# Optimization experiments

Hardware: AMD Instinct MI355X
Metric: run time of the kernel (lower is better)

The kernel has to match this reference:

```python
import jax, jax.numpy as jnp
import numpy as np

D_MODEL = 1024


def pos_encoding(seq_len, d_model):
    # pos: [S,1], i: [d/2]
    pos = jnp.arange(seq_len, dtype=jnp.float32)[:, None]
    i = jnp.arange(0, d_model, 2, dtype=jnp.float32)
    angle_rates = 1.0 / jnp.power(10000.0, i / d_model)
    angle_rads = pos * angle_rates  # [S, d/2]
    # NOTE: original concatenates sin block then cos block (not interleaved)
    return jnp.concatenate([jnp.sin(angle_rads), jnp.cos(angle_rads)], axis=-1)  # [S, d]


def setup_inputs() -> dict:
    key = jax.random.key(0)
    ks = jax.random.split(key, 4)
    B, S, D = 4, 2048, D_MODEL
    scale = 1.0 / np.sqrt(D)
    x = jax.random.normal(ks[0], (B, S, D), dtype=jnp.float32)
    Wq = jax.random.normal(ks[1], (D, D), dtype=jnp.float32) * scale
    Wk = jax.random.normal(ks[2], (D, D), dtype=jnp.float32) * scale
    Wv = jax.random.normal(ks[3], (D, D), dtype=jnp.float32) * scale
    bq = jnp.zeros((D,), dtype=jnp.float32)
    bk = jnp.zeros((D,), dtype=jnp.float32)
    bv = jnp.zeros((D,), dtype=jnp.float32)
    return {"x": x, "Wq": Wq, "bq": bq, "Wk": Wk, "bk": bk, "Wv": Wv, "bv": bv}


def reference(x, Wq, bq, Wk, bk, Wv, bv):
    B, S, D = x.shape
    pe = pos_encoding(S, D)  # [S, D]
    h = x + pe[None, :, :]
    q = jnp.einsum('bsd,de->bse', h, Wq) + bq
    k = jnp.einsum('bsd,de->bse', h, Wk) + bk
    v = jnp.einsum('bsd,de->bse', h, Wv) + bv
    logits = jnp.einsum('bqd,bkd->bqk', q, k) / jnp.sqrt(jnp.float32(D))
    attn = jax.nn.softmax(logits, axis=-1)
    out = jnp.einsum('bqk,bkd->bqd', attn, v)
    return x + out
```

## Files before the change

kernel.cpp:

```cpp
#include <hip/hip_runtime.h>
#include <stdint.h>


#define AS1(p) ((__attribute__((address_space(1))) void*)(p))
#define AS3(p) ((__attribute__((address_space(3))) void*)(p))

typedef _Float16 f16x8 __attribute__((ext_vector_type(8)));
typedef _Float16 f16x4 __attribute__((ext_vector_type(4)));
typedef float f32x4 __attribute__((ext_vector_type(4)));

__global__ __launch_bounds__(256) void prep(const float* __restrict__ x,
                                            _Float16* __restrict__ h,
                                            const float* __restrict__ Wq,
                                            const float* __restrict__ Wk,
                                            const float* __restrict__ Wv,
                                            _Float16* __restrict__ Wt,
                                            float* __restrict__ rowsum) {
  const int bx = blockIdx.x;
  const int tid = threadIdx.x;
  if (bx < 8192) {
    const size_t e = ((size_t)bx * 256 + tid) * 4;
    const int d = (int)(e & 1023);
    const int s = (int)((e >> 10) & 2047);
    const float4 xv = *(const float4*)(x + e);
    const int half = d >> 9;
    const int j0 = d & 511;
    const float c = -0.017988946039016f;
    f16x4 o;
#pragma unroll
    for (int t = 0; t < 4; t++) {
      const float r = __expf((float)(j0 + t) * c);
      const float a = (float)s * r;
      const float p = half ? __cosf(a) : __sinf(a);
      const float xe = (t == 0) ? xv.x : (t == 1) ? xv.y : (t == 2) ? xv.z : xv.w;
      o[t] = (_Float16)(xe + p);
    }
    *(f16x4*)(h + e) = o;
  } else if (bx < 11264) {
    __shared__ float t[32][33];
    const int w = bx - 8192;
    const int z = w >> 10;
    const int rem = w & 1023;
    const int n0 = (rem & 31) * 32, k0 = (rem >> 5) * 32;
    const float* W = (z == 0) ? Wq : (z == 1) ? Wk : Wv;
    _Float16* o = Wt + (size_t)z * 1048576;
    const int tx = tid & 31, ty = tid >> 5;
#pragma unroll
    for (int i = ty; i < 32; i += 8)
      t[i][tx] = W[(size_t)(k0 + i) * 1024 + (n0 + tx)];
    __syncthreads();
#pragma unroll
    for (int i = ty; i < 32; i += 8)
      o[(size_t)(n0 + i) * 1024 + (k0 + tx)] = (_Float16)t[tx][i];
  } else {
    rowsum[(bx - 11264) * 256 + tid] = 0.f;
  }
}

#define RD_A(SET, S_)                                                         \
  {                                                                           \
    _Pragma("unroll") for (int fi = 0; fi < 4; fi++)                          \
      _Pragma("unroll") for (int kk = 0; kk < 2; kk++)                        \
        SET[fi * 2 + kk] = *(const f16x8*)&As[bb][kk][                        \
            (wr * 128 + (S_) * 64 + fi * 16 + l16) * 32 + quad * 8];          \
  }
#define RD_B(SET, S_)                                                         \
  {                                                                           \
    _Pragma("unroll") for (int fj = 0; fj < 2; fj++)                          \
      _Pragma("unroll") for (int kk = 0; kk < 2; kk++)                        \
        SET[fj * 2 + kk] = *(const f16x8*)&Bs[bb][kk][                        \
            (wc * 64 + (S_) * 32 + fj * 16 + l16) * 32 + quad * 8];           \
  }
#define MFMA16(ASET, BSET, MQ, NQ)                                            \
  {                                                                           \
    __builtin_amdgcn_s_setprio(1);                                            \
    _Pragma("unroll") for (int fi = 0; fi < 4; fi++)                          \
      _Pragma("unroll") for (int fj = 0; fj < 2; fj++)                        \
        _Pragma("unroll") for (int kk = 0; kk < 2; kk++)                      \
          acc[(MQ) * 4 + fi][(NQ) * 2 + fj] =                                 \
              __builtin_amdgcn_mfma_f32_16x16x32_f16(                         \
                  ASET[fi * 2 + kk], BSET[fj * 2 + kk],                       \
                  acc[(MQ) * 4 + fi][(NQ) * 2 + fj], 0, 0, 0);                \
    __builtin_amdgcn_s_setprio(0);                                            \
  }
#define PHASE_WAIT()                                                          \
  __builtin_amdgcn_s_barrier();                                               \
  asm volatile("s_waitcnt lgkmcnt(0)" ::: "memory");                          \
  __builtin_amdgcn_sched_barrier(0);

template <int MODE>
__global__ __launch_bounds__(512) void gemm256(
    const _Float16* __restrict__ A0, long long sA,
    const _Float16* __restrict__ B0, long long sB,
    void* __restrict__ C0, long long sC,
    const float* __restrict__ aux0, const float* __restrict__ aux1,
    const float* __restrict__ aux2, float* __restrict__ rowsum,
    _Float16* __restrict__ vT, const int K, const int N, const int ldc) {
  __shared__ __align__(16) _Float16 As[2][2][8192];
  __shared__ __align__(16) _Float16 Bs[2][2][8192];
  const int tid = threadIdx.x;
  const int bid = blockIdx.x;

  int z, bm0, bn0;
  if (MODE == 0) {
    const int w = (bid & 7) * 48 + (bid >> 3);
    const int m = w / 12, r = w - m * 12;
    z = r >> 2; bn0 = (r & 3) * 256; bm0 = m * 256;
  } else {
    const int w = (bid & 7) * 32 + (bid >> 3);
    z = w >> 6;
    const int r = w & 63;
    bm0 = (r >> 3) * 256; bn0 = (r & 7) * 256;
  }
  const _Float16* A = A0 + (size_t)z * sA;
  const _Float16* Bt = B0 + (size_t)z * sB;

  const _Float16* aS = A + (size_t)(bm0 + (tid >> 2)) * K + (tid & 3) * 8;
  const _Float16* bS = Bt + (size_t)(bn0 + (tid >> 2)) * K + (tid & 3) * 8;
  const size_t halfStep = (size_t)128 * K;

  auto stageA = [&](int X, int h) {
    const int b = X & 1;
    const _Float16* s = aS + (size_t)X * 64 + (size_t)h * halfStep;
    _Float16* d = &As[b][0][h * 4096 + tid * 8];
    __builtin_amdgcn_global_load_lds(AS1(s), AS3(d), 16, 0, 0);
    __builtin_amdgcn_global_load_lds(AS1(s + 32), AS3(d + 8192), 16, 0, 0);
  };
  auto stageB = [&](int X, int h) {
    const int b = X & 1;
    const _Float16* s = bS + (size_t)X * 64 + (size_t)h * halfStep;
    _Float16* d = &Bs[b][0][h * 4096 + tid * 8];
    __builtin_amdgcn_global_load_lds(AS1(s), AS3(d), 16, 0, 0);
    __builtin_amdgcn_global_load_lds(AS1(s + 32), AS3(d + 8192), 16, 0, 0);
  };

  const int lane = tid & 63, wave = tid >> 6;
  const int wr = wave >> 2, wc = wave & 3;
  const int quad = lane >> 4, l16 = lane & 15;

  f32x4 acc[8][4];
#pragma unroll
  for (int i = 0; i < 8; i++)
#pragma unroll
    for (int j = 0; j < 4; j++) {
      f32x4 zz = {0.f, 0.f, 0.f, 0.f};
      acc[i][j] = zz;
    }

  const int nt = K >> 6;

  stageA(0, 0); stageA(0, 1); stageB(0, 0); stageB(0, 1);
  stageA(1, 0); stageA(1, 1);
  asm volatile("s_waitcnt vmcnt(4)" ::: "memory");
  __builtin_amdgcn_s_barrier();

  f16x8 a0[8], a1[8], b0f[4], b1f[4];

  for (int T = 0; T < nt; ++T) {
    const int bb = T & 1;
    RD_A(a0, 0);
    RD_B(b0f, 0);
    if (T + 1 < nt) stageB(T + 1, 0);
    PHASE_WAIT();
    MFMA16(a0, b0f, 0, 0);
    __builtin_amdgcn_s_barrier();
    RD_A(a1, 1);
    if (T + 1 < nt) stageB(T + 1, 1);
    PHASE_WAIT();
    MFMA16(a1, b0f, 1, 0);
    __builtin_amdgcn_s_barrier();
    RD_B(b1f, 1);
    if (T + 2 < nt) stageA(T + 2, 0);
    PHASE_WAIT();
    MFMA16(a0, b1f, 0, 1);
    __builtin_amdgcn_s_barrier();
    if (T + 2 < nt) stageA(T + 2, 1);
    PHASE_WAIT();
    MFMA16(a1, b1f, 1, 1);
    if (T + 1 < nt) {
      if (T + 2 < nt) asm volatile("s_waitcnt vmcnt(4)" ::: "memory");
      else            asm volatile("s_waitcnt vmcnt(0)" ::: "memory");
      __builtin_amdgcn_s_barrier();
    }
  }

  const int rowb = bm0 + wr * 128 + quad * 4;
  const int colb = bn0 + wc * 64 + l16;
  if (MODE == 0) {
    const float* bias = (z == 0) ? aux0 : (z == 1) ? aux1 : aux2;
    if (z == 2) {
      const int b_ = rowb >> 11, sl = rowb & 2047;
      _Float16* vb = vT + (size_t)b_ * 2097152;
#pragma unroll
      for (int i = 0; i < 8; i++)
#pragma unroll
        for (int j = 0; j < 4; j++) {
          const int gn = colb + j * 16;
          const float bb2 = bias[gn];
          f16x4 o;
#pragma unroll
          for (int r = 0; r < 4; r++) o[r] = (_Float16)(acc[i][j][r] + bb2);
          *(f16x4*)&vb[(size_t)gn * 2048 + sl + i * 16] = o;
        }
    } else {
      _Float16* C = (_Float16*)C0 + (size_t)z * sC;
#pragma unroll
      for (int i = 0; i < 8; i++)
#pragma unroll
        for (int j = 0; j < 4; j++) {
          const int gn = colb + j * 16;
          const float bb2 = bias[gn];
#pragma unroll
          for (int r = 0; r < 4; r++)
            C[(size_t)(rowb + i * 16 + r) * N + gn] = (_Float16)(acc[i][j][r] + bb2);
        }
    }
  } else {
    _Float16* C = (_Float16*)C0 + (size_t)z * sC;
    float rs[4] = {0.f, 0.f, 0.f, 0.f};
#pragma unroll
    for (int i = 0; i < 8; i++)
#pragma unroll
      for (int j = 0; j < 4; j++) {
        const int gn = colb + j * 16;
        f16x4 o;
        float pj = 0.f;
#pragma unroll
        for (int r = 0; r < 4; r++) {
          const float e = __expf(acc[i][j][r] * 0.03125f);
          o[r] = (_Float16)e;
          pj += e;
        }
        rs[j] += pj;
        *(f16x4*)&C[(size_t)gn * ldc + rowb + i * 16] = o;
      }
#pragma unroll
    for (int j = 0; j < 4; j++) {
      float v = rs[j];
      v += __shfl_xor(v, 16);
      v += __shfl_xor(v, 32);
      if (quad == 0) atomicAdd(&rowsum[z * 2048 + colb + j * 16], v);
    }
  }
}

__global__ __launch_bounds__(256) void gemm_pv(
    const _Float16* __restrict__ A0, long long sA,
    const _Float16* __restrict__ B0, long long sB,
    float* __restrict__ C0, long long sC,
    const float* __restrict__ X0, const float* __restrict__ rowsum,
    long long sX, const int K, const int ldc) {
  __shared__ __align__(16) _Float16 As[4 * 4096];
  __shared__ __align__(16) _Float16 Bs[4 * 4096];
  const int tid = threadIdx.x;
  const int bid = blockIdx.x;

  const int c = bid & 7, t0 = bid >> 3;
  const int zx = (t0 & 3) * 8 + c;
  const int y = t0 >> 2;
  const int z = zx >> 3;
  const int bm0 = (zx & 7) * 128, bn0 = y * 128;

  const _Float16* A = A0 + (size_t)z * sA;
  const _Float16* Bt = B0 + (size_t)z * sB;

  const _Float16* a0 = A + (size_t)(bm0 + (tid >> 2)) * K + (tid & 3) * 8;
  const _Float16* a1 = a0 + (size_t)64 * K;
  const _Float16* b0 = Bt + (size_t)(bn0 + (tid >> 2)) * K + (tid & 3) * 8;
  const _Float16* b1 = b0 + (size_t)64 * K;

  auto stage = [&](int s) {
    const int r = s & 3;
    const int k = s * 32;
    __builtin_amdgcn_global_load_lds(AS1(a0 + k), AS3(&As[r * 4096 + tid * 8]), 16, 0, 0);
    __builtin_amdgcn_global_load_lds(AS1(a1 + k), AS3(&As[r * 4096 + tid * 8 + 2048]), 16, 0, 0);
    __builtin_amdgcn_global_load_lds(AS1(b0 + k), AS3(&Bs[r * 4096 + tid * 8]), 16, 0, 0);
    __builtin_amdgcn_global_load_lds(AS1(b1 + k), AS3(&Bs[r * 4096 + tid * 8 + 2048]), 16, 0, 0);
  };

  const int lane = tid & 63, wave = tid >> 6;
  const int wr = wave >> 1, wc = wave & 1;
  const int quad = lane >> 4, l16 = lane & 15;

  f32x4 acc[4][4];
#pragma unroll
  for (int i = 0; i < 4; i++)
#pragma unroll
    for (int j = 0; j < 4; j++) {
      f32x4 zz = {0.f, 0.f, 0.f, 0.f};
      acc[i][j] = zz;
    }

  const int NS = K >> 5;

  stage(0); stage(1); stage(2);
  asm volatile("s_waitcnt vmcnt(8)" ::: "memory");
  __builtin_amdgcn_s_barrier();

  for (int s = 0; s < NS; ++s) {
    const int r = s & 3;
    f16x8 af[4], bf[4];
#pragma unroll
    for (int i = 0; i < 4; i++)
      af[i] = *(const f16x8*)&As[r * 4096 + (wr * 64 + i * 16 + l16) * 32 + quad * 8];
#pragma unroll
    for (int j = 0; j < 4; j++)
      bf[j] = *(const f16x8*)&Bs[r * 4096 + (wc * 64 + j * 16 + l16) * 32 + quad * 8];
    if (s + 3 < NS) stage(s + 3);
    __builtin_amdgcn_s_barrier();
    asm volatile("s_waitcnt lgkmcnt(0)" ::: "memory");
    __builtin_amdgcn_sched_barrier(0);
    __builtin_amdgcn_s_setprio(1);
#pragma unroll
    for (int i = 0; i < 4; i++)
#pragma unroll
      for (int j = 0; j < 4; j++)
        acc[i][j] = __builtin_amdgcn_mfma_f32_16x16x32_f16(af[i], bf[j],
                                                           acc[i][j], 0, 0, 0);
    __builtin_amdgcn_s_setprio(0);
    __builtin_amdgcn_sched_barrier(0);
    if (s + 1 < NS) {
      if (s + 3 < NS)       asm volatile("s_waitcnt vmcnt(8)" ::: "memory");
      else if (s + 3 == NS) asm volatile("s_waitcnt vmcnt(4)" ::: "memory");
      else                  asm volatile("s_waitcnt vmcnt(0)" ::: "memory");
      __builtin_amdgcn_s_barrier();
    }
  }

  const int rowb = bm0 + wr * 64 + quad * 4;
  const int colb = bn0 + wc * 64 + l16;
  float* C = C0 + (size_t)z * sC;
  const float* X = X0 + (size_t)z * sX;
  float inv[4];
#pragma unroll
  for (int j = 0; j < 4; j++)
    inv[j] = 1.0f / rowsum[z * 2048 + colb + j * 16];
#pragma unroll
  for (int i = 0; i < 4; i++)
#pragma unroll
    for (int j = 0; j < 4; j++) {
      const int gn = colb + j * 16;
      const size_t base = (size_t)gn * ldc + rowb + i * 16;
      const float4 xv = *(const float4*)(X + base);
      float4 o;
      o.x = acc[i][j][0] * inv[j] + xv.x;
      o.y = acc[i][j][1] * inv[j] + xv.y;
      o.z = acc[i][j][2] * inv[j] + xv.z;
      o.w = acc[i][j][3] * inv[j] + xv.w;
      *(float4*)(C + base) = o;
    }
}

extern "C" void kernel_launch(void* const* d_in, const int* in_sizes, int n_in,
                              void* d_out, int out_size, void* d_ws, size_t ws_size,
                              hipStream_t stream) {
  (void)in_sizes; (void)n_in; (void)out_size; (void)ws_size;
  const float* x  = (const float*)d_in[0];
  const float* Wq = (const float*)d_in[1];
  const float* bq = (const float*)d_in[2];
  const float* Wk = (const float*)d_in[3];
  const float* bk = (const float*)d_in[4];
  const float* Wv = (const float*)d_in[5];
  const float* bv = (const float*)d_in[6];
  float* out = (float*)d_out;
  char* ws = (char*)d_ws;

  _Float16* h    = (_Float16*)(ws);
  _Float16* Wt   = (_Float16*)(ws + 16777216);
  _Float16* qkv  = (_Float16*)(ws + 23068672);
  _Float16* attn = (_Float16*)(ws + 73400320);
  float* rowsum  = (float*)   (ws + 106954752);

  const long long E = 8388608;
  _Float16* vT = qkv + 2 * E;

  prep<<<11296, 256, 0, stream>>>(x, h, Wq, Wk, Wv, Wt, rowsum);

  gemm256<0><<<384, 512, 0, stream>>>(
      h, 0LL, Wt, 1048576LL, qkv, E, bq, bk, bv, nullptr, vT,
      1024, 1024, 0);

  gemm256<1><<<256, 512, 0, stream>>>(
      qkv + E, 2097152LL, qkv, 2097152LL, attn, 4194304LL,
      nullptr, nullptr, nullptr, rowsum, nullptr,
      1024, 2048, 2048);

  gemm_pv<<<512, 256, 0, stream>>>(
      vT, 2097152LL, attn, 4194304LL, out, 2097152LL,
      x, rowsum, 2097152LL, 2048, 1024);
}
```

Before: 265.1 us.

## Replace QKV projection GEMM with dedicated 256x128-tile kernel using triple-buffered LDS

The QKV projection now runs in its own kernel with 256-thread blocks, 256x128 output tiles and a three-stage global-to-LDS ring buffer, launched as 768 blocks instead of 384 blocks of 512 threads with 256x256 tiles. The templated kernel is specialised to the logits-only path, and gemm_pv is moved without functional change. The aim is better occupancy and load balance across CUs on the projection GEMM. In exchange, each block reuses each loaded tile less and the new kernel drops the phased sub-tile pipelining of the old one.

```diff
diff --git a/kernel.cpp b/kernel.cpp
--- a/kernel.cpp
+++ b/kernel.cpp
@@ -57,6 +57,225 @@
   }
 }
 
+__global__ __launch_bounds__(256) void gemm_qkv(
+    const _Float16* __restrict__ A0, const _Float16* __restrict__ B0,
+    _Float16* __restrict__ qk, const float* __restrict__ bq,
+    const float* __restrict__ bk, const float* __restrict__ bv,
+    _Float16* __restrict__ vT) {
+  constexpr int K = 1024;
+  __shared__ __align__(16) _Float16 As[3 * 8192];
+  __shared__ __align__(16) _Float16 Bs[3 * 4096];
+  const int tid = threadIdx.x;
+  const int bid = blockIdx.x;
+
+  const int w = (bid & 7) * 96 + (bid >> 3);
+  const int m = w / 24, r = w - m * 24;
+  const int z = r >> 3, n = r & 7;
+  const int bm0 = m * 256, bn0 = n * 128;
+
+  const _Float16* Bt = B0 + (size_t)z * 1048576;
+  const _Float16* aS = A0 + (size_t)(bm0 + (tid >> 2)) * K + (tid & 3) * 8;
+  const _Float16* bS = Bt + (size_t)(bn0 + (tid >> 2)) * K + (tid & 3) * 8;
+
+  auto stage = [&](int kt, int ra, int rb2) {
+    const int k = kt * 32;
+    __builtin_amdgcn_global_load_lds(AS1(aS + k), AS3(&As[ra + tid * 8]), 16, 0, 0);
+    __builtin_amdgcn_global_load_lds(AS1(aS + k + 64 * K), AS3(&As[ra + tid * 8 + 2048]), 16, 0, 0);
+    __builtin_amdgcn_global_load_lds(AS1(aS + k + 128 * K), AS3(&As[ra + tid * 8 + 4096]), 16, 0, 0);
+    __builtin_amdgcn_global_load_lds(AS1(aS + k + 192 * K), AS3(&As[ra + tid * 8 + 6144]), 16, 0, 0);
+    __builtin_amdgcn_global_load_lds(AS1(bS + k), AS3(&Bs[rb2 + tid * 8]), 16, 0, 0);
+    __builtin_amdgcn_global_load_lds(AS1(bS + k + 64 * K), AS3(&Bs[rb2 + tid * 8 + 2048]), 16, 0, 0);
+  };
+
+  const int lane = tid & 63, wave = tid >> 6;
+  const int wr = wave >> 1, wc = wave & 1;
+  const int quad = lane >> 4, l16 = lane & 15;
+
+  f32x4 acc[8][4];
+#pragma unroll
+  for (int i = 0; i < 8; i++)
+#pragma unroll
+    for (int j = 0; j < 4; j++) {
+      f32x4 zz = {0.f, 0.f, 0.f, 0.f};
+      acc[i][j] = zz;
+    }
+
+  const int NS = K >> 5;
+
+  stage(0, 0, 0);
+  stage(1, 8192, 4096);
+  asm volatile("s_waitcnt vmcnt(6)" ::: "memory");
+  __builtin_amdgcn_s_barrier();
+
+  int rA = 0, rB = 0;
+  int sA = 16384, sB = 8192;
+  for (int s = 0; s < NS; ++s) {
+    if (s + 2 < NS) stage(s + 2, sA, sB);
+    f16x8 af[8], bf[4];
+#pragma unroll
+    for (int i = 0; i < 8; i++)
+      af[i] = *(const f16x8*)&As[rA + (wr * 128 + i * 16 + l16) * 32 + quad * 8];
+#pragma unroll
+    for (int j = 0; j < 4; j++)
+      bf[j] = *(const f16x8*)&Bs[rB + (wc * 64 + j * 16 + l16) * 32 + quad * 8];
+    __builtin_amdgcn_s_setprio(1);
+#pragma unroll
+    for (int i = 0; i < 8; i++)
+#pragma unroll
+      for (int j = 0; j < 4; j++)
+        acc[i][j] = __builtin_amdgcn_mfma_f32_16x16x32_f16(af[i], bf[j],
+                                                           acc[i][j], 0, 0, 0);
+    __builtin_amdgcn_s_setprio(0);
+    if (s + 1 < NS) {
+      if (s + 2 < NS) asm volatile("s_waitcnt vmcnt(6)" ::: "memory");
+      else            asm volatile("s_waitcnt vmcnt(0)" ::: "memory");
+      __builtin_amdgcn_s_barrier();
+    }
+    rA = (rA == 16384) ? 0 : rA + 8192;
+    rB = (rB == 8192) ? 0 : rB + 4096;
+    sA = (sA == 16384) ? 0 : sA + 8192;
+    sB = (sB == 8192) ? 0 : sB + 4096;
+  }
+
+  const int rowb = bm0 + wr * 128 + quad * 4;
+  const int colb = bn0 + wc * 64 + l16;
+  const float* bias = (z == 0) ? bq : (z == 1) ? bk : bv;
+  if (z == 2) {
+    const int b = rowb >> 11, sl = rowb & 2047;
+    _Float16* vb = vT + (size_t)b * 2097152;
+#pragma unroll
+    for (int i = 0; i < 8; i++)
+#pragma unroll
+      for (int j = 0; j < 4; j++) {
+        const int gn = colb + j * 16;
+        const float bb = bias[gn];
+        f16x4 o;
+#pragma unroll
+        for (int rr = 0; rr < 4; rr++) o[rr] = (_Float16)(acc[i][j][rr] + bb);
+        *(f16x4*)&vb[(size_t)gn * 2048 + sl + i * 16] = o;
+      }
+  } else {
+    _Float16* C = qk + (size_t)z * 8388608;
+#pragma unroll
+    for (int i = 0; i < 8; i++)
+#pragma unroll
+      for (int j = 0; j < 4; j++) {
+        const int gn = colb + j * 16;
+        const float bb = bias[gn];
+#pragma unroll
+        for (int rr = 0; rr < 4; rr++)
+          C[(size_t)(rowb + i * 16 + rr) * 1024 + gn] = (_Float16)(acc[i][j][rr] + bb);
+      }
+  }
+}
+
+__global__ __launch_bounds__(256) void gemm_pv(
+    const _Float16* __restrict__ A0, long long sA,
+    const _Float16* __restrict__ B0, long long sB,
+    float* __restrict__ C0, long long sC,
+    const float* __restrict__ X0, const float* __restrict__ rowsum,
+    long long sX, const int K, const int ldc) {
+  __shared__ __align__(16) _Float16 As[4 * 4096];
+  __shared__ __align__(16) _Float16 Bs[4 * 4096];
+  const int tid = threadIdx.x;
+  const int bid = blockIdx.x;
+
+  const int c = bid & 7, t0 = bid >> 3;
+  const int zx = (t0 & 3) * 8 + c;
+  const int y = t0 >> 2;
+  const int z = zx >> 3;
+  const int bm0 = (zx & 7) * 128, bn0 = y * 128;
+
+  const _Float16* A = A0 + (size_t)z * sA;
+  const _Float16* Bt = B0 + (size_t)z * sB;
+
+  const _Float16* a0 = A + (size_t)(bm0 + (tid >> 2)) * K + (tid & 3) * 8;
+  const _Float16* a1 = a0 + (size_t)64 * K;
+  const _Float16* b0 = Bt + (size_t)(bn0 + (tid >> 2)) * K + (tid & 3) * 8;
+  const _Float16* b1 = b0 + (size_t)64 * K;
+
+  auto stage = [&](int s) {
+    const int r = s & 3;
+    const int k = s * 32;
+    __builtin_amdgcn_global_load_lds(AS1(a0 + k), AS3(&As[r * 4096 + tid * 8]), 16, 0, 0);
+    __builtin_amdgcn_global_load_lds(AS1(a1 + k), AS3(&As[r * 4096 + tid * 8 + 2048]), 16, 0, 0);
+    __builtin_amdgcn_global_load_lds(AS1(b0 + k), AS3(&Bs[r * 4096 + tid * 8]), 16, 0, 0);
+    __builtin_amdgcn_global_load_lds(AS1(b1 + k), AS3(&Bs[r * 4096 + tid * 8 + 2048]), 16, 0, 0);
+  };
+
+  const int lane = tid & 63, wave = tid >> 6;
+  const int wr = wave >> 1, wc = wave & 1;
+  const int quad = lane >> 4, l16 = lane & 15;
+
+  f32x4 acc[4][4];
+#pragma unroll
+  for (int i = 0; i < 4; i++)
+#pragma unroll
+    for (int j = 0; j < 4; j++) {
+      f32x4 zz = {0.f, 0.f, 0.f, 0.f};
+      acc[i][j] = zz;
+    }
+
+  const int NS = K >> 5;
+
+  stage(0); stage(1); stage(2);
+  asm volatile("s_waitcnt vmcnt(8)" ::: "memory");
+  __builtin_amdgcn_s_barrier();
+
+  for (int s = 0; s < NS; ++s) {
+    const int r = s & 3;
+    f16x8 af[4], bf[4];
+#pragma unroll
+    for (int i = 0; i < 4; i++)
+      af[i] = *(const f16x8*)&As[r * 4096 + (wr * 64 + i * 16 + l16) * 32 + quad * 8];
+#pragma unroll
+    for (int j = 0; j < 4; j++)
+      bf[j] = *(const f16x8*)&Bs[r * 4096 + (wc * 64 + j * 16 + l16) * 32 + quad * 8];
+    if (s + 3 < NS) stage(s + 3);
+    __builtin_amdgcn_s_barrier();
+    asm volatile("s_waitcnt lgkmcnt(0)" ::: "memory");
+    __builtin_amdgcn_sched_barrier(0);
+    __builtin_amdgcn_s_setprio(1);
+#pragma unroll
+    for (int i = 0; i < 4; i++)
+#pragma unroll
+      for (int j = 0; j < 4; j++)
+        acc[i][j] = __builtin_amdgcn_mfma_f32_16x16x32_f16(af[i], bf[j],
+                                                           acc[i][j], 0, 0, 0);
+    __builtin_amdgcn_s_setprio(0);
+    __builtin_amdgcn_sched_barrier(0);
+    if (s + 1 < NS) {
+      if (s + 3 < NS)       asm volatile("s_waitcnt vmcnt(8)" ::: "memory");
+      else if (s + 3 == NS) asm volatile("s_waitcnt vmcnt(4)" ::: "memory");
+      else                  asm volatile("s_waitcnt vmcnt(0)" ::: "memory");
+      __builtin_amdgcn_s_barrier();
+    }
+  }
+
+  const int rowb = bm0 + wr * 64 + quad * 4;
+  const int colb = bn0 + wc * 64 + l16;
+  float* C = C0 + (size_t)z * sC;
+  const float* X = X0 + (size_t)z * sX;
+  float inv[4];
+#pragma unroll
+  for (int j = 0; j < 4; j++)
+    inv[j] = 1.0f / rowsum[z * 2048 + colb + j * 16];
+#pragma unroll
+  for (int i = 0; i < 4; i++)
+#pragma unroll
+    for (int j = 0; j < 4; j++) {
+      const int gn = colb + j * 16;
+      const size_t base = (size_t)gn * ldc + rowb + i * 16;
+      const float4 xv = *(const float4*)(X + base);
+      float4 o;
+      o.x = acc[i][j][0] * inv[j] + xv.x;
+      o.y = acc[i][j][1] * inv[j] + xv.y;
+      o.z = acc[i][j][2] * inv[j] + xv.z;
+      o.w = acc[i][j][3] * inv[j] + xv.w;
+      *(float4*)(C + base) = o;
+    }
+}
+
 #define RD_A(SET, S_)                                                         \
   {                                                                           \
     _Pragma("unroll") for (int fi = 0; fi < 4; fi++)                          \
@@ -88,30 +307,21 @@
   asm volatile("s_waitcnt lgkmcnt(0)" ::: "memory");                          \
   __builtin_amdgcn_sched_barrier(0);
 
-template <int MODE>
-__global__ __launch_bounds__(512) void gemm256(
+__global__ __launch_bounds__(512) void gemm256_logits(
     const _Float16* __restrict__ A0, long long sA,
     const _Float16* __restrict__ B0, long long sB,
     void* __restrict__ C0, long long sC,
-    const float* __restrict__ aux0, const float* __restrict__ aux1,
-    const float* __restrict__ aux2, float* __restrict__ rowsum,
-    _Float16* __restrict__ vT, const int K, const int N, const int ldc) {
+    float* __restrict__ rowsum, const int K, const int ldc) {
   __shared__ __align__(16) _Float16 As[2][2][8192];
   __shared__ __align__(16) _Float16 Bs[2][2][8192];
   const int tid = threadIdx.x;
   const int bid = blockIdx.x;
 
-  int z, bm0, bn0;
-  if (MODE == 0) {
-    const int w = (bid & 7) * 48 + (bid >> 3);
-    const int m = w / 12, r = w - m * 12;
-    z = r >> 2; bn0 = (r & 3) * 256; bm0 = m * 256;
-  } else {
-    const int w = (bid & 7) * 32 + (bid >> 3);
-    z = w >> 6;
-    const int r = w & 63;
-    bm0 = (r >> 3) * 256; bn0 = (r & 7) * 256;
-  }
+  const int w = (bid & 7) * 32 + (bid >> 3);
+  const int z = w >> 6;
+  const int r0 = w & 63;
+  const int bm0 = (r0 >> 3) * 256, bn0 = (r0 & 7) * 256;
+
   const _Float16* A = A0 + (size_t)z * sA;
   const _Float16* Bt = B0 + (size_t)z * sB;
 
@@ -186,169 +396,31 @@
 
   const int rowb = bm0 + wr * 128 + quad * 4;
   const int colb = bn0 + wc * 64 + l16;
-  if (MODE == 0) {
-    const float* bias = (z == 0) ? aux0 : (z == 1) ? aux1 : aux2;
-    if (z == 2) {
-      const int b_ = rowb >> 11, sl = rowb & 2047;
-      _Float16* vb = vT + (size_t)b_ * 2097152;
-#pragma unroll
-      for (int i = 0; i < 8; i++)
-#pragma unroll
-        for (int j = 0; j < 4; j++) {
-          const int gn = colb + j * 16;
-          const float bb2 = bias[gn];
-          f16x4 o;
-#pragma unroll
-          for (int r = 0; r < 4; r++) o[r] = (_Float16)(acc[i][j][r] + bb2);
-          *(f16x4*)&vb[(size_t)gn * 2048 + sl + i * 16] = o;
-        }
-    } else {
-      _Float16* C = (_Float16*)C0 + (size_t)z * sC;
-#pragma unroll
-      for (int i = 0; i < 8; i++)
-#pragma unroll
-        for (int j = 0; j < 4; j++) {
-          const int gn = colb + j * 16;
-          const float bb2 = bias[gn];
-#pragma unroll
-          for (int r = 0; r < 4; r++)
-            C[(size_t)(rowb + i * 16 + r) * N + gn] = (_Float16)(acc[i][j][r] + bb2);
-        }
-    }
-  } else {
-    _Float16* C = (_Float16*)C0 + (size_t)z * sC;
-    float rs[4] = {0.f, 0.f, 0.f, 0.f};
-#pragma unroll
-    for (int i = 0; i < 8; i++)
-#pragma unroll
-      for (int j = 0; j < 4; j++) {
-        const int gn = colb + j * 16;
-        f16x4 o;
-        float pj = 0.f;
-#pragma unroll
-        for (int r = 0; r < 4; r++) {
-          const float e = __expf(acc[i][j][r] * 0.03125f);
-          o[r] = (_Float16)e;
-          pj += e;
-        }
-        rs[j] += pj;
-        *(f16x4*)&C[(size_t)gn * ldc + rowb + i * 16] = o;
-      }
-#pragma unroll
-    for (int j = 0; j < 4; j++) {
-      float v = rs[j];
-      v += __shfl_xor(v, 16);
-      v += __shfl_xor(v, 32);
-      if (quad == 0) atomicAdd(&rowsum[z * 2048 + colb + j * 16], v);
-    }
-  }
-}
-
-__global__ __launch_bounds__(256) void gemm_pv(
-    const _Float16* __restrict__ A0, long long sA,
-    const _Float16* __restrict__ B0, long long sB,
-    float* __restrict__ C0, long long sC,
-    const float* __restrict__ X0, const float* __restrict__ rowsum,
-    long long sX, const int K, const int ldc) {
-  __shared__ __align__(16) _Float16 As[4 * 4096];
-  __shared__ __align__(16) _Float16 Bs[4 * 4096];
-  const int tid = threadIdx.x;
-  const int bid = blockIdx.x;
-
-  const int c = bid & 7, t0 = bid >> 3;
-  const int zx = (t0 & 3) * 8 + c;
-  const int y = t0 >> 2;
-  const int z = zx >> 3;
-  const int bm0 = (zx & 7) * 128, bn0 = y * 128;
-
-  const _Float16* A = A0 + (size_t)z * sA;
-  const _Float16* Bt = B0 + (size_t)z * sB;
-
-  const _Float16* a0 = A + (size_t)(bm0 + (tid >> 2)) * K + (tid & 3) * 8;
-  const _Float16* a1 = a0 + (size_t)64 * K;
-  const _Float16* b0 = Bt + (size_t)(bn0 + (tid >> 2)) * K + (tid & 3) * 8;
-  const _Float16* b1 = b0 + (size_t)64 * K;
-
-  auto stage = [&](int s) {
-    const int r = s & 3;
-    const int k = s * 32;
-    __builtin_amdgcn_global_load_lds(AS1(a0 + k), AS3(&As[r * 4096 + tid * 8]), 16, 0, 0);
-    __builtin_amdgcn_global_load_lds(AS1(a1 + k), AS3(&As[r * 4096 + tid * 8 + 2048]), 16, 0, 0);
-    __builtin_amdgcn_global_load_lds(AS1(b0 + k), AS3(&Bs[r * 4096 + tid * 8]), 16, 0, 0);
-    __builtin_amdgcn_global_load_lds(AS1(b1 + k), AS3(&Bs[r * 4096 + tid * 8 + 2048]), 16, 0, 0);
-  };
-
-  const int lane = tid & 63, wave = tid >> 6;
-  const int wr = wave >> 1, wc = wave & 1;
-  const int quad = lane >> 4, l16 = lane & 15;
-
-  f32x4 acc[4][4];
-#pragma unroll
-  for (int i = 0; i < 4; i++)
-#pragma unroll
-    for (int j = 0; j < 4; j++) {
-      f32x4 zz = {0.f, 0.f, 0.f, 0.f};
-      acc[i][j] = zz;
-    }
-
-  const int NS = K >> 5;
-
-  stage(0); stage(1); stage(2);
-  asm volatile("s_waitcnt vmcnt(8)" ::: "memory");
-  __builtin_amdgcn_s_barrier();
-
-  for (int s = 0; s < NS; ++s) {
-    const int r = s & 3;
-    f16x8 af[4], bf[4];
-#pragma unroll
-    for (int i = 0; i < 4; i++)
-      af[i] = *(const f16x8*)&As[r * 4096 + (wr * 64 + i * 16 + l16) * 32 + quad * 8];
-#pragma unroll
-    for (int j = 0; j < 4; j++)
-      bf[j] = *(const f16x8*)&Bs[r * 4096 + (wc * 64 + j * 16 + l16) * 32 + quad * 8];
-    if (s + 3 < NS) stage(s + 3);
-    __builtin_amdgcn_s_barrier();
-    asm volatile("s_waitcnt lgkmcnt(0)" ::: "memory");
-    __builtin_amdgcn_sched_barrier(0);
-    __builtin_amdgcn_s_setprio(1);
-#pragma unroll
-    for (int i = 0; i < 4; i++)
-#pragma unroll
-      for (int j = 0; j < 4; j++)
-        acc[i][j] = __builtin_amdgcn_mfma_f32_16x16x32_f16(af[i], bf[j],
-                                                           acc[i][j], 0, 0, 0);
-    __builtin_amdgcn_s_setprio(0);
-    __builtin_amdgcn_sched_barrier(0);
-    if (s + 1 < NS) {
-      if (s + 3 < NS)       asm volatile("s_waitcnt vmcnt(8)" ::: "memory");
-      else if (s + 3 == NS) asm volatile("s_waitcnt vmcnt(4)" ::: "memory");
-      else                  asm volatile("s_waitcnt vmcnt(0)" ::: "memory");
-      __builtin_amdgcn_s_barrier();
-    }
-  }
-
-  const int rowb = bm0 + wr * 64 + quad * 4;
-  const int colb = bn0 + wc * 64 + l16;
-  float* C = C0 + (size_t)z * sC;
-  const float* X = X0 + (size_t)z * sX;
-  float inv[4];
-#pragma unroll
-  for (int j = 0; j < 4; j++)
-    inv[j] = 1.0f / rowsum[z * 2048 + colb + j * 16];
-#pragma unroll
-  for (int i = 0; i < 4; i++)
+  _Float16* C = (_Float16*)C0 + (size_t)z * sC;
+  float rs[4] = {0.f, 0.f, 0.f, 0.f};
+#pragma unroll
+  for (int i = 0; i < 8; i++)
 #pragma unroll
     for (int j = 0; j < 4; j++) {
       const int gn = colb + j * 16;
-      const size_t base = (size_t)gn * ldc + rowb + i * 16;
-      const float4 xv = *(const float4*)(X + base);
-      float4 o;
-      o.x = acc[i][j][0] * inv[j] + xv.x;
-      o.y = acc[i][j][1] * inv[j] + xv.y;
-      o.z = acc[i][j][2] * inv[j] + xv.z;
-      o.w = acc[i][j][3] * inv[j] + xv.w;
-      *(float4*)(C + base) = o;
-    }
+      f16x4 o;
+      float pj = 0.f;
+#pragma unroll
+      for (int r = 0; r < 4; r++) {
+        const float e = __expf(acc[i][j][r] * 0.03125f);
+        o[r] = (_Float16)e;
+        pj += e;
+      }
+      rs[j] += pj;
+      *(f16x4*)&C[(size_t)gn * ldc + rowb + i * 16] = o;
+    }
+#pragma unroll
+  for (int j = 0; j < 4; j++) {
+    float v = rs[j];
+    v += __shfl_xor(v, 16);
+    v += __shfl_xor(v, 32);
+    if (quad == 0) atomicAdd(&rowsum[z * 2048 + colb + j * 16], v);
+  }
 }
 
 extern "C" void kernel_launch(void* const* d_in, const int* in_sizes, int n_in,
@@ -376,14 +448,11 @@
 
   prep<<<11296, 256, 0, stream>>>(x, h, Wq, Wk, Wv, Wt, rowsum);
 
-  gemm256<0><<<384, 512, 0, stream>>>(
-      h, 0LL, Wt, 1048576LL, qkv, E, bq, bk, bv, nullptr, vT,
-      1024, 1024, 0);
-
-  gemm256<1><<<256, 512, 0, stream>>>(
+  gemm_qkv<<<768, 256, 0, stream>>>(h, Wt, qkv, bq, bk, bv, vT);
+
+  gemm256_logits<<<256, 512, 0, stream>>>(
       qkv + E, 2097152LL, qkv, 2097152LL, attn, 4194304LL,
-      nullptr, nullptr, nullptr, rowsum, nullptr,
-      1024, 2048, 2048);
+      rowsum, 1024, 2048);
 
   gemm_pv<<<512, 256, 0, stream>>>(
       vT, 2097152LL, attn, 4194304LL, out, 2097152LL,
```

New measurement: 310.5 us. 17.1% more time.
